# Kernel tuning notes

Hardware: AMD Instinct MI355X
Metric: run time of the kernel (lower is better)

The kernel has to match this reference:

```python
import jax, jax.numpy as jnp
import numpy as np

S, L, E, H, V, T, A = 4096, 16, 512, 512, 100000, 64, 50


def setup_inputs() -> dict:
    key = jax.random.key(0)
    ks = jax.random.split(key, 20)
    f32 = jnp.float32
    n = lambda k, shape: jax.random.normal(k, shape, f32) * 0.05
    return {
        "sent_in": jax.random.randint(ks[0], (S,), 0, V),
        "char_in": jax.random.randint(ks[1], (S, L), 0, A),
        "lengths": jax.random.randint(ks[2], (S,), 1, L + 1),
        "word_emb": n(ks[3], (V, E)),
        "char_emb": n(ks[4], (A, E)),
        "Wih_w": n(ks[5], (4 * H, E)),
        "Whh_w": n(ks[6], (4 * H, H)),
        "bih_w": n(ks[7], (4 * H,)),
        "bhh_w": n(ks[8], (4 * H,)),
        "Wih_c": n(ks[9], (4 * H, E)),
        "Whh_c": n(ks[10], (4 * H, H)),
        "bih_c": n(ks[11], (4 * H,)),
        "bhh_c": n(ks[12], (4 * H,)),
        "Ww2t": n(ks[13], (T, H)),
        "bw2t": n(ks[14], (T,)),
        "Wc2t": n(ks[15], (T, H)),
        "bc2t": n(ks[16], (T,)),
    }


def _lstm(xs, mask, W_ih, W_hh, b_ih, b_hh):
    """xs: [T, B, E], mask: [T, B] (1 = valid). Returns hs: [T, B, H].
    PyTorch gate order i, f, g, o. Carry is frozen on masked steps."""
    Hd = W_hh.shape[1]
    B = xs.shape[1]
    gx = jnp.einsum('tbe,ge->tbg', xs, W_ih) + b_ih  # precompute input gates

    def step(carry, inp):
        h, c = carry
        g, m = inp
        gates = g + h @ W_hh.T + b_hh
        i, f, gg, o = jnp.split(gates, 4, axis=-1)
        c_new = jax.nn.sigmoid(f) * c + jax.nn.sigmoid(i) * jnp.tanh(gg)
        h_new = jax.nn.sigmoid(o) * jnp.tanh(c_new)
        mm = m[:, None]
        h_new = jnp.where(mm, h_new, h)
        c_new = jnp.where(mm, c_new, c)
        return (h_new, c_new), h_new

    h0 = jnp.zeros((B, Hd), xs.dtype)
    c0 = jnp.zeros((B, Hd), xs.dtype)
    _, hs = jax.lax.scan(step, (h0, c0), (gx, mask))
    return hs


def reference(sent_in, char_in, lengths, word_emb, char_emb,
              Wih_w, Whh_w, bih_w, bhh_w,
              Wih_c, Whh_c, bih_c, bhh_c,
              Ww2t, bw2t, Wc2t, bc2t):
    # word-level LSTM over the sentence (batch = 1)
    xs_w = word_emb[sent_in][:, None, :]                  # [S, 1, E]
    mask_w = jnp.ones((sent_in.shape[0], 1), jnp.bool_)
    hs_w = _lstm(xs_w, mask_w, Wih_w, Whh_w, bih_w, bhh_w)  # [S, 1, H]
    word_scores = hs_w[:, 0, :] @ Ww2t.T + bw2t           # [S, T]

    # char-level LSTM: all words processed as one batch, masked by length
    xs_c = char_emb[char_in].transpose(1, 0, 2)           # [L, S, E]
    Lm = char_in.shape[1]
    mask_c = jnp.arange(Lm)[:, None] < lengths[None, :]   # [L, S]
    hs_c = _lstm(xs_c, mask_c, Wih_c, Whh_c, bih_c, bhh_c)  # [L, S, H]
    out_sum = jnp.sum(hs_c * mask_c[:, :, None].astype(hs_c.dtype), axis=0)  # [S, H]
    char_scores = out_sum @ Wc2t.T + bc2t                 # [S, T]

    return jax.nn.log_softmax(char_scores + word_scores, axis=1)
```

## Files before the change

kernel.cpp:

```cpp
#include <hip/hip_runtime.h>
#include <cstdint>
#include <cstddef>

#define S_  4096
#define L_  16
#define E_  512
#define H_  512
#define G4_ 2048
#define T_  64
#define WORD_WGS 32
#define CHAR_WGS 256
#define ALL_WGS  (WORD_WGS + CHAR_WGS)

__device__ __forceinline__ float sigmoidf_(float x) {
    return 1.0f / (1.0f + __expf(-x));
}
__device__ __forceinline__ float fast_tanhf_(float x) {
    return 1.0f - 2.0f / (__expf(2.0f * x) + 1.0f);
}

#define BM 128
#define BN 128
#define BK 16

__global__ __launch_bounds__(256, 2)
void gemm_nt_kernel(const float* __restrict__ A1, const int* __restrict__ idxA,
                    int idxStride, int idxOff, const float* __restrict__ A2,
                    const float* __restrict__ B1, const float* __restrict__ B2,
                    int Ksplit, int K, int N, float* __restrict__ C)
{
    __shared__ float As_[BK][BM + 4];
    __shared__ float Bs_[BK][BN + 4];
    __shared__ int   rIdx_[BM];

    const int tid = threadIdx.x;
    const int m0 = blockIdx.y * BM;
    const int n0 = blockIdx.x * BN;
    if (idxA && tid < BM)
        rIdx_[tid] = idxA[(size_t)(m0 + tid) * idxStride + idxOff];

    const int tx = tid & 15;
    const int ty = tid >> 4;
    const int ar = tid >> 2;
    const int aq = tid & 3;

    float acc[8][8];
#pragma unroll
    for (int i = 0; i < 8; ++i)
#pragma unroll
        for (int j = 0; j < 8; ++j) acc[i][j] = 0.f;

    for (int k0 = 0; k0 < K; k0 += BK) {
        __syncthreads();
        const bool firstHalf = (k0 < Ksplit);
        const int  kk0 = firstHalf ? k0 : (k0 - Ksplit);
#pragma unroll
        for (int part = 0; part < 2; ++part) {
            const int row = ar + part * 64;
            float4 av, bv;
            if (firstHalf) {
                const int grA = idxA ? rIdx_[row] : (m0 + row);
                av = *(const float4*)(A1 + (size_t)grA * Ksplit + kk0 + aq * 4);
                bv = *(const float4*)(B1 + (size_t)(n0 + row) * Ksplit + kk0 + aq * 4);
            } else {
                const int Kr = K - Ksplit;
                av = *(const float4*)(A2 + (size_t)(m0 + row) * Kr + kk0 + aq * 4);
                bv = *(const float4*)(B2 + (size_t)(n0 + row) * Kr + kk0 + aq * 4);
            }
            As_[aq * 4 + 0][row] = av.x; As_[aq * 4 + 1][row] = av.y;
            As_[aq * 4 + 2][row] = av.z; As_[aq * 4 + 3][row] = av.w;
            Bs_[aq * 4 + 0][row] = bv.x; Bs_[aq * 4 + 1][row] = bv.y;
            Bs_[aq * 4 + 2][row] = bv.z; Bs_[aq * 4 + 3][row] = bv.w;
        }
        __syncthreads();
#pragma unroll
        for (int kk = 0; kk < BK; ++kk) {
            const float4 a0 = *(const float4*)&As_[kk][ty * 4];
            const float4 a1 = *(const float4*)&As_[kk][64 + ty * 4];
            const float4 b0 = *(const float4*)&Bs_[kk][tx * 4];
            const float4 b1 = *(const float4*)&Bs_[kk][64 + tx * 4];
            const float a[8] = {a0.x, a0.y, a0.z, a0.w, a1.x, a1.y, a1.z, a1.w};
            const float b[8] = {b0.x, b0.y, b0.z, b0.w, b1.x, b1.y, b1.z, b1.w};
#pragma unroll
            for (int i = 0; i < 8; ++i)
#pragma unroll
                for (int j = 0; j < 8; ++j)
                    acc[i][j] = fmaf(a[i], b[j], acc[i][j]);
        }
    }
#pragma unroll
    for (int ri = 0; ri < 2; ++ri)
#pragma unroll
        for (int i = 0; i < 4; ++i) {
            const int m = m0 + ri * 64 + ty * 4 + i;
            float4 v0 = make_float4(acc[ri * 4 + i][0], acc[ri * 4 + i][1],
                                    acc[ri * 4 + i][2], acc[ri * 4 + i][3]);
            float4 v1 = make_float4(acc[ri * 4 + i][4], acc[ri * 4 + i][5],
                                    acc[ri * 4 + i][6], acc[ri * 4 + i][7]);
            *(float4*)(C + (size_t)m * N + n0 + tx * 4)      = v0;
            *(float4*)(C + (size_t)m * N + n0 + 64 + tx * 4) = v1;
        }
}

__global__ __launch_bounds__(512, 4)
void fused_lstm_kernel(const float* __restrict__ gxw,
                       const float* __restrict__ Whh_w,
                       const float* __restrict__ bih_w,
                       const float* __restrict__ bhh_w,
                       float* __restrict__ hsw, float* __restrict__ h_buf,
                       unsigned int* __restrict__ cnt,
                       const int* __restrict__ char_in,
                       const int* __restrict__ lengths,
                       const float* __restrict__ char_emb,
                       const float* __restrict__ Wih_c,
                       const float* __restrict__ Whh_c,
                       const float* __restrict__ bih_c,
                       const float* __restrict__ bhh_c,
                       float* __restrict__ h_c, float* __restrict__ c_c,
                       float* __restrict__ osum)
{
    __shared__ float h_lds[512];
    __shared__ float gate_lds[64];
    __shared__ float wb[64];
    __shared__ float As[16][132];
    __shared__ float Bs[16][260];
    __shared__ int   rIdx[128];
    __shared__ int   lens[128];
    __shared__ float cb[256];

    const int tid = threadIdx.x;

    if (blockIdx.x < WORD_WGS) {
        const int wg   = blockIdx.x;
        const int base = wg * 16;
        const int r    = tid >> 3;
        const int p    = tid & 7;
        const int grow = (r >> 4) * 512 + base + (r & 15);

        float wreg[64];
        {
            const float4* Wrow = (const float4*)(Whh_w + (size_t)grow * 512);
#pragma unroll
            for (int kk = 0; kk < 16; ++kk) {
                const float4 v = Wrow[kk * 8 + p];
                wreg[kk * 4 + 0] = v.x; wreg[kk * 4 + 1] = v.y;
                wreg[kk * 4 + 2] = v.z; wreg[kk * 4 + 3] = v.w;
            }
#pragma unroll
            for (int i = 0; i < 64; ++i) asm volatile("" : "+v"(wreg[i]));
        }
        if (tid < 64) {
            const int gr = (tid >> 4) * 512 + base + (tid & 15);
            wb[tid] = bih_w[gr] + bhh_w[gr];
        }
        if (tid < 128) ((float4*)h_lds)[tid] = make_float4(0.f, 0.f, 0.f, 0.f);
        float cstate = 0.f;
        __syncthreads();

        float gxv = (p == 0) ? gxw[grow] : 0.f;
        for (int t = 0; t < S_; ++t) {
            float gxn = 0.f;
            if (p == 0 && t + 1 < S_) gxn = gxw[(size_t)(t + 1) * G4_ + grow];

            float s = 0.f;
#pragma unroll
            for (int kk = 0; kk < 16; ++kk) {
                const float4 h4 = ((const float4*)h_lds)[kk * 8 + p];
                s = fmaf(wreg[kk * 4 + 0], h4.x, s);
                s = fmaf(wreg[kk * 4 + 1], h4.y, s);
                s = fmaf(wreg[kk * 4 + 2], h4.z, s);
                s = fmaf(wreg[kk * 4 + 3], h4.w, s);
            }
            s += __shfl_xor(s, 1);
            s += __shfl_xor(s, 2);
            s += __shfl_xor(s, 4);
            if (p == 0) gate_lds[r] = s + gxv + wb[r];
            __syncthreads();

            if (tid < 16) {
                const float gi = gate_lds[tid];
                const float gf = gate_lds[16 + tid];
                const float gg = gate_lds[32 + tid];
                const float go = gate_lds[48 + tid];
                const float cn = sigmoidf_(gf) * cstate + sigmoidf_(gi) * fast_tanhf_(gg);
                cstate = cn;
                const float hn = sigmoidf_(go) * fast_tanhf_(cn);
                hsw[(size_t)t * H_ + base + tid] = hn;
                __hip_atomic_store(&h_buf[((t + 1) & 1) * H_ + base + tid], hn,
                                   __ATOMIC_RELAXED, __HIP_MEMORY_SCOPE_AGENT);
            }
            __syncthreads();

            if (tid == 0) {
                __hip_atomic_fetch_add(&cnt[0], 1u, __ATOMIC_RELEASE,
                                       __HIP_MEMORY_SCOPE_AGENT);
                while (__hip_atomic_load(&cnt[0], __ATOMIC_ACQUIRE,
                                         __HIP_MEMORY_SCOPE_AGENT)
                       < (unsigned)WORD_WGS * (unsigned)(t + 1))
                    __builtin_amdgcn_s_sleep(2);
            }
            __syncthreads();

            h_lds[tid] = __hip_atomic_load(&h_buf[((t + 1) & 1) * H_ + tid],
                                           __ATOMIC_RELAXED, __HIP_MEMORY_SCOPE_AGENT);
            __syncthreads();
            gxv = gxn;
        }
    } else {
        const int cw  = blockIdx.x - WORD_WGS;
        const int m0  = (cw >> 3) * 128;
        const int hu0 = (cw & 7) * 64;
        const int tx  = tid & 31;
        const int ty  = tid >> 5;

        if (tid < 128) lens[tid] = lengths[m0 + tid];
        if (tid < 256) {
            const int g = tid >> 6, ul = tid & 63;
            const int br = g * 512 + hu0 + ul;
            cb[tid] = bih_c[br] + bhh_c[br];
        }

        for (int l = 0; l < L_; ++l) {
            if (tid < 128) rIdx[tid] = char_in[(size_t)(m0 + tid) * L_ + l];

            float acc[8][8];
#pragma unroll
            for (int i = 0; i < 8; ++i)
#pragma unroll
                for (int j = 0; j < 8; ++j) acc[i][j] = 0.f;

            for (int kt = 0; kt < 64; ++kt) {
                const int k0 = kt * 16;
                __syncthreads();
                const int row = tid >> 2, q = tid & 3;
                float4 av;
                if (k0 < 512) {
                    av = *(const float4*)(char_emb + (size_t)rIdx[row] * E_ + k0 + q * 4);
                } else {
                    const float* hp = h_c + (size_t)(m0 + row) * H_ + (k0 - 512) + q * 4;
                    av.x = __hip_atomic_load(hp + 0, __ATOMIC_RELAXED, __HIP_MEMORY_SCOPE_AGENT);
                    av.y = __hip_atomic_load(hp + 1, __ATOMIC_RELAXED, __HIP_MEMORY_SCOPE_AGENT);
                    av.z = __hip_atomic_load(hp + 2, __ATOMIC_RELAXED, __HIP_MEMORY_SCOPE_AGENT);
                    av.w = __hip_atomic_load(hp + 3, __ATOMIC_RELAXED, __HIP_MEMORY_SCOPE_AGENT);
                }
                As[q * 4 + 0][row] = av.x; As[q * 4 + 1][row] = av.y;
                As[q * 4 + 2][row] = av.z; As[q * 4 + 3][row] = av.w;
#pragma unroll
                for (int cc = 0; cc < 2; ++cc) {
                    const int c  = row + cc * 128;
                    const int g  = c >> 6, u = c & 63;
                    const int br = g * 512 + hu0 + u;
                    const float* bp = (k0 < 512)
                        ? (Wih_c + (size_t)br * E_ + k0 + q * 4)
                        : (Whh_c + (size_t)br * H_ + (k0 - 512) + q * 4);
                    const float4 bv = *(const float4*)bp;
                    Bs[q * 4 + 0][c] = bv.x; Bs[q * 4 + 1][c] = bv.y;
                    Bs[q * 4 + 2][c] = bv.z; Bs[q * 4 + 3][c] = bv.w;
                }
                __syncthreads();
#pragma unroll
                for (int kk = 0; kk < 16; ++kk) {
                    const float4 a0 = *(const float4*)&As[kk][ty * 8];
                    const float4 a1 = *(const float4*)&As[kk][ty * 8 + 4];
                    const float a[8] = {a0.x, a0.y, a0.z, a0.w, a1.x, a1.y, a1.z, a1.w};
                    float b[8];
#pragma unroll
                    for (int g = 0; g < 4; ++g) {
                        const float2 bg = *(const float2*)&Bs[kk][g * 64 + 2 * tx];
                        b[(g << 1)]     = bg.x;
                        b[(g << 1) | 1] = bg.y;
                    }
#pragma unroll
                    for (int i = 0; i < 8; ++i)
#pragma unroll
                        for (int j = 0; j < 8; ++j)
                            acc[i][j] = fmaf(a[i], b[j], acc[i][j]);
                }
            }

            __syncthreads();
            if (tid == 0) {
                __hip_atomic_fetch_add(&cnt[32], 1u, __ATOMIC_RELEASE,
                                       __HIP_MEMORY_SCOPE_AGENT);
                while (__hip_atomic_load(&cnt[32], __ATOMIC_ACQUIRE,
                                         __HIP_MEMORY_SCOPE_AGENT)
                       < (unsigned)CHAR_WGS * (unsigned)(2 * l + 1))
                    __builtin_amdgcn_s_sleep(2);
            }
            __syncthreads();

#pragma unroll
            for (int i = 0; i < 8; ++i) {
                const int mr = ty * 8 + i;
                const int m  = m0 + mr;
                if (l < lens[mr]) {
                    const int hl = 2 * tx;
                    float* cp = c_c  + (size_t)m * H_ + hu0 + hl;
                    float* op = osum + (size_t)m * H_ + hu0 + hl;
                    float2 c2 = *(float2*)cp;
                    float2 o2 = *(float2*)op;
#pragma unroll
                    for (int u = 0; u < 2; ++u) {
                        const float I = sigmoidf_(acc[i][0 + u] + cb[      hl + u]);
                        const float F = sigmoidf_(acc[i][2 + u] + cb[ 64 + hl + u]);
                        const float G = fast_tanhf_(acc[i][4 + u] + cb[128 + hl + u]);
                        const float O = sigmoidf_(acc[i][6 + u] + cb[192 + hl + u]);
                        const float cv = u ? c2.y : c2.x;
                        const float cn = F * cv + I * G;
                        const float hn = O * fast_tanhf_(cn);
                        if (u) { c2.y = cn; o2.y += hn; } else { c2.x = cn; o2.x += hn; }
                        __hip_atomic_store(h_c + (size_t)m * H_ + hu0 + hl + u, hn,
                                           __ATOMIC_RELAXED, __HIP_MEMORY_SCOPE_AGENT);
                    }
                    *(float2*)cp = c2;
                    *(float2*)op = o2;
                }
            }

            __syncthreads();
            if (tid == 0) {
                __hip_atomic_fetch_add(&cnt[32], 1u, __ATOMIC_RELEASE,
                                       __HIP_MEMORY_SCOPE_AGENT);
                while (__hip_atomic_load(&cnt[32], __ATOMIC_ACQUIRE,
                                         __HIP_MEMORY_SCOPE_AGENT)
                       < (unsigned)CHAR_WGS * (unsigned)(2 * l + 2))
                    __builtin_amdgcn_s_sleep(2);
            }
            __syncthreads();
        }
    }
}

__global__ __launch_bounds__(64)
void scores_kernel(const float* __restrict__ hsw, const float* __restrict__ osum,
                   const float* __restrict__ Ww2t, const float* __restrict__ bw2t,
                   const float* __restrict__ Wc2t, const float* __restrict__ bc2t,
                   float* __restrict__ out)
{
    const int s = blockIdx.x;
    const int t = threadIdx.x;
    __shared__ float4 hrow[128], orow[128];
    hrow[t]      = ((const float4*)(hsw + (size_t)s * H_))[t];
    hrow[t + 64] = ((const float4*)(hsw + (size_t)s * H_))[t + 64];
    orow[t]      = ((const float4*)(osum + (size_t)s * H_))[t];
    orow[t + 64] = ((const float4*)(osum + (size_t)s * H_))[t + 64];
    __syncthreads();

    float acc = bw2t[t] + bc2t[t];
    const float4* w1 = (const float4*)(Ww2t + (size_t)t * H_);
    const float4* w2 = (const float4*)(Wc2t + (size_t)t * H_);
#pragma unroll 8
    for (int k = 0; k < 128; ++k) {
        const float4 a = w1[k], hb = hrow[k];
        acc = fmaf(a.x, hb.x, acc); acc = fmaf(a.y, hb.y, acc);
        acc = fmaf(a.z, hb.z, acc); acc = fmaf(a.w, hb.w, acc);
        const float4 b = w2[k], ob = orow[k];
        acc = fmaf(b.x, ob.x, acc); acc = fmaf(b.y, ob.y, acc);
        acc = fmaf(b.z, ob.z, acc); acc = fmaf(b.w, ob.w, acc);
    }
    float m = acc;
#pragma unroll
    for (int off = 32; off > 0; off >>= 1) m = fmaxf(m, __shfl_xor(m, off));
    float sum = __expf(acc - m);
#pragma unroll
    for (int off = 32; off > 0; off >>= 1) sum += __shfl_xor(sum, off);
    out[(size_t)s * T_ + t] = acc - m - __logf(sum);
}

extern "C" void kernel_launch(void* const* d_in, const int* in_sizes, int n_in,
                              void* d_out, int out_size, void* d_ws, size_t ws_size,
                              hipStream_t stream)
{
    (void)in_sizes; (void)n_in; (void)out_size; (void)ws_size;

    const int*   sent_in  = (const int*)d_in[0];
    const int*   char_in  = (const int*)d_in[1];
    const int*   lengths  = (const int*)d_in[2];
    const float* word_emb = (const float*)d_in[3];
    const float* char_emb = (const float*)d_in[4];
    const float* Wih_w    = (const float*)d_in[5];
    const float* Whh_w    = (const float*)d_in[6];
    const float* bih_w    = (const float*)d_in[7];
    const float* bhh_w    = (const float*)d_in[8];
    const float* Wih_c    = (const float*)d_in[9];
    const float* Whh_c    = (const float*)d_in[10];
    const float* bih_c    = (const float*)d_in[11];
    const float* bhh_c    = (const float*)d_in[12];
    const float* Ww2t     = (const float*)d_in[13];
    const float* bw2t     = (const float*)d_in[14];
    const float* Wc2t     = (const float*)d_in[15];
    const float* bc2t     = (const float*)d_in[16];

    char* ws = (char*)d_ws;
    float* gxw  = (float*)(ws + 0);
    float* hsw  = (float*)(ws + 33554432);
    float* h_c  = (float*)(ws + 41943040);
    float* c_c  = (float*)(ws + 50331648);
    float* osum = (float*)(ws + 58720256);
    float* hbuf = (float*)(ws + 67108864);
    unsigned int* cnt = (unsigned int*)(ws + 67112960);

    hipMemsetAsync(hbuf, 0, 4096, stream);
    hipMemsetAsync(cnt,  0, 16384, stream);
    hipMemsetAsync(h_c,  0, 8388608, stream);
    hipMemsetAsync(c_c,  0, 8388608, stream);
    hipMemsetAsync(osum, 0, 8388608, stream);

    const dim3 gemmGrid(G4_ / BN, S_ / BM);
    gemm_nt_kernel<<<gemmGrid, 256, 0, stream>>>(
        word_emb, sent_in, 1, 0, nullptr,
        Wih_w, nullptr, E_, E_, G4_, gxw);

    fused_lstm_kernel<<<ALL_WGS, 512, 0, stream>>>(
        gxw, Whh_w, bih_w, bhh_w, hsw, hbuf, cnt,
        char_in, lengths, char_emb, Wih_c, Whh_c, bih_c, bhh_c,
        h_c, c_c, osum);

    scores_kernel<<<S_, 64, 0, stream>>>(hsw, osum, Ww2t, bw2t, Wc2t, bc2t,
                                         (float*)d_out);
}
```

Measured before the change: 14.88 ms.

## Spread word LSTM over 128 workgroups with per-workgroup flag barrier

```diff
diff --git a/kernel.cpp b/kernel.cpp
--- a/kernel.cpp
+++ b/kernel.cpp
@@ -8,8 +8,8 @@
 #define H_  512
 #define G4_ 2048
 #define T_  64
-#define WORD_WGS 32
-#define CHAR_WGS 256
+#define WORD_WGS 128
+#define CHAR_WGS 128
 #define ALL_WGS  (WORD_WGS + CHAR_WGS)
 
 __device__ __forceinline__ float sigmoidf_(float x) {
@@ -25,9 +25,9 @@
 
 __global__ __launch_bounds__(256, 2)
 void gemm_nt_kernel(const float* __restrict__ A1, const int* __restrict__ idxA,
-                    int idxStride, int idxOff, const float* __restrict__ A2,
-                    const float* __restrict__ B1, const float* __restrict__ B2,
-                    int Ksplit, int K, int N, float* __restrict__ C)
+                    int idxStride, int idxOff,
+                    const float* __restrict__ B1, int K, int N,
+                    float* __restrict__ C)
 {
     __shared__ float As_[BK][BM + 4];
     __shared__ float Bs_[BK][BN + 4];
@@ -36,7 +36,7 @@
     const int tid = threadIdx.x;
     const int m0 = blockIdx.y * BM;
     const int n0 = blockIdx.x * BN;
-    if (idxA && tid < BM)
+    if (tid < BM)
         rIdx_[tid] = idxA[(size_t)(m0 + tid) * idxStride + idxOff];
 
     const int tx = tid & 15;
@@ -52,21 +52,12 @@
 
     for (int k0 = 0; k0 < K; k0 += BK) {
         __syncthreads();
-        const bool firstHalf = (k0 < Ksplit);
-        const int  kk0 = firstHalf ? k0 : (k0 - Ksplit);
 #pragma unroll
         for (int part = 0; part < 2; ++part) {
             const int row = ar + part * 64;
-            float4 av, bv;
-            if (firstHalf) {
-                const int grA = idxA ? rIdx_[row] : (m0 + row);
-                av = *(const float4*)(A1 + (size_t)grA * Ksplit + kk0 + aq * 4);
-                bv = *(const float4*)(B1 + (size_t)(n0 + row) * Ksplit + kk0 + aq * 4);
-            } else {
-                const int Kr = K - Ksplit;
-                av = *(const float4*)(A2 + (size_t)(m0 + row) * Kr + kk0 + aq * 4);
-                bv = *(const float4*)(B2 + (size_t)(n0 + row) * Kr + kk0 + aq * 4);
-            }
+            const int grA = rIdx_[row];
+            float4 av = *(const float4*)(A1 + (size_t)grA * K + k0 + aq * 4);
+            float4 bv = *(const float4*)(B1 + (size_t)(n0 + row) * K + k0 + aq * 4);
             As_[aq * 4 + 0][row] = av.x; As_[aq * 4 + 1][row] = av.y;
             As_[aq * 4 + 2][row] = av.z; As_[aq * 4 + 3][row] = av.w;
             Bs_[aq * 4 + 0][row] = bv.x; Bs_[aq * 4 + 1][row] = bv.y;
@@ -119,101 +110,111 @@
                        float* __restrict__ h_c, float* __restrict__ c_c,
                        float* __restrict__ osum)
 {
-    __shared__ float h_lds[512];
-    __shared__ float gate_lds[64];
-    __shared__ float wb[64];
-    __shared__ float As[16][132];
-    __shared__ float Bs[16][260];
-    __shared__ int   rIdx[128];
-    __shared__ int   lens[128];
-    __shared__ float cb[256];
-
+    __shared__ __align__(16) unsigned char smem[27392];
     const int tid = threadIdx.x;
 
     if (blockIdx.x < WORD_WGS) {
+        float* h_lds    = (float*)smem;
+        float* gate_lds = (float*)(smem + 2048);
+        float* wb       = (float*)(smem + 2112);
+
         const int wg   = blockIdx.x;
-        const int base = wg * 16;
-        const int r    = tid >> 3;
-        const int p    = tid & 7;
-        const int grow = (r >> 4) * 512 + base + (r & 15);
-
-        float wreg[64];
+        const int base = wg * 4;
+        const int r    = tid >> 5;
+        const int p    = tid & 31;
+        const int grow = (r >> 2) * 512 + base + (r & 3);
+
+        float4 w0, w1, w2, w3;
         {
             const float4* Wrow = (const float4*)(Whh_w + (size_t)grow * 512);
-#pragma unroll
-            for (int kk = 0; kk < 16; ++kk) {
-                const float4 v = Wrow[kk * 8 + p];
-                wreg[kk * 4 + 0] = v.x; wreg[kk * 4 + 1] = v.y;
-                wreg[kk * 4 + 2] = v.z; wreg[kk * 4 + 3] = v.w;
-            }
-#pragma unroll
-            for (int i = 0; i < 64; ++i) asm volatile("" : "+v"(wreg[i]));
-        }
-        if (tid < 64) {
-            const int gr = (tid >> 4) * 512 + base + (tid & 15);
+            w0 = Wrow[p];       w1 = Wrow[32 + p];
+            w2 = Wrow[64 + p];  w3 = Wrow[96 + p];
+        }
+        if (tid < 16) {
+            const int gr = (tid >> 2) * 512 + base + (tid & 3);
             wb[tid] = bih_w[gr] + bhh_w[gr];
         }
         if (tid < 128) ((float4*)h_lds)[tid] = make_float4(0.f, 0.f, 0.f, 0.f);
         float cstate = 0.f;
         __syncthreads();
 
+        unsigned int* flags = cnt + 64;
         float gxv = (p == 0) ? gxw[grow] : 0.f;
+
         for (int t = 0; t < S_; ++t) {
             float gxn = 0.f;
             if (p == 0 && t + 1 < S_) gxn = gxw[(size_t)(t + 1) * G4_ + grow];
 
+            const float4* h4 = (const float4*)h_lds;
+            float4 ha = h4[p], hb = h4[32 + p], hc = h4[64 + p], hd = h4[96 + p];
             float s = 0.f;
-#pragma unroll
-            for (int kk = 0; kk < 16; ++kk) {
-                const float4 h4 = ((const float4*)h_lds)[kk * 8 + p];
-                s = fmaf(wreg[kk * 4 + 0], h4.x, s);
-                s = fmaf(wreg[kk * 4 + 1], h4.y, s);
-                s = fmaf(wreg[kk * 4 + 2], h4.z, s);
-                s = fmaf(wreg[kk * 4 + 3], h4.w, s);
-            }
+            s = fmaf(w0.x, ha.x, s); s = fmaf(w0.y, ha.y, s);
+            s = fmaf(w0.z, ha.z, s); s = fmaf(w0.w, ha.w, s);
+            s = fmaf(w1.x, hb.x, s); s = fmaf(w1.y, hb.y, s);
+            s = fmaf(w1.z, hb.z, s); s = fmaf(w1.w, hb.w, s);
+            s = fmaf(w2.x, hc.x, s); s = fmaf(w2.y, hc.y, s);
+            s = fmaf(w2.z, hc.z, s); s = fmaf(w2.w, hc.w, s);
+            s = fmaf(w3.x, hd.x, s); s = fmaf(w3.y, hd.y, s);
+            s = fmaf(w3.z, hd.z, s); s = fmaf(w3.w, hd.w, s);
+            s += __shfl_xor(s, 16);
+            s += __shfl_xor(s, 8);
+            s += __shfl_xor(s, 4);
+            s += __shfl_xor(s, 2);
             s += __shfl_xor(s, 1);
-            s += __shfl_xor(s, 2);
-            s += __shfl_xor(s, 4);
             if (p == 0) gate_lds[r] = s + gxv + wb[r];
             __syncthreads();
 
-            if (tid < 16) {
-                const float gi = gate_lds[tid];
-                const float gf = gate_lds[16 + tid];
-                const float gg = gate_lds[32 + tid];
-                const float go = gate_lds[48 + tid];
-                const float cn = sigmoidf_(gf) * cstate + sigmoidf_(gi) * fast_tanhf_(gg);
-                cstate = cn;
-                const float hn = sigmoidf_(go) * fast_tanhf_(cn);
-                hsw[(size_t)t * H_ + base + tid] = hn;
-                __hip_atomic_store(&h_buf[((t + 1) & 1) * H_ + base + tid], hn,
-                                   __ATOMIC_RELAXED, __HIP_MEMORY_SCOPE_AGENT);
+            if (tid < 64) {
+                if (tid < 4) {
+                    const float gi = gate_lds[tid];
+                    const float gf = gate_lds[4 + tid];
+                    const float gg = gate_lds[8 + tid];
+                    const float go = gate_lds[12 + tid];
+                    const float cn = sigmoidf_(gf) * cstate
+                                   + sigmoidf_(gi) * fast_tanhf_(gg);
+                    cstate = cn;
+                    const float hn = sigmoidf_(go) * fast_tanhf_(cn);
+                    hsw[(size_t)t * H_ + base + tid] = hn;
+                    __hip_atomic_store(&h_buf[((t + 1) & 1) * H_ + base + tid],
+                                       hn, __ATOMIC_RELAXED,
+                                       __HIP_MEMORY_SCOPE_AGENT);
+                }
+                if (tid == 0)
+                    __hip_atomic_store(&flags[wg * 16],
+                                       (unsigned int)(t + 1), __ATOMIC_RELEASE,
+                                       __HIP_MEMORY_SCOPE_AGENT);
+                const unsigned int tp1 = (unsigned int)(t + 1);
+                for (;;) {
+                    unsigned int f1 = __hip_atomic_load(
+                        &flags[tid * 16], __ATOMIC_ACQUIRE,
+                        __HIP_MEMORY_SCOPE_AGENT);
+                    unsigned int f2 = __hip_atomic_load(
+                        &flags[(64 + tid) * 16], __ATOMIC_ACQUIRE,
+                        __HIP_MEMORY_SCOPE_AGENT);
+                    if (__all((int)(f1 >= tp1 && f2 >= tp1))) break;
+                    __builtin_amdgcn_s_sleep(1);
+                }
             }
             __syncthreads();
-
-            if (tid == 0) {
-                __hip_atomic_fetch_add(&cnt[0], 1u, __ATOMIC_RELEASE,
-                                       __HIP_MEMORY_SCOPE_AGENT);
-                while (__hip_atomic_load(&cnt[0], __ATOMIC_ACQUIRE,
-                                         __HIP_MEMORY_SCOPE_AGENT)
-                       < (unsigned)WORD_WGS * (unsigned)(t + 1))
-                    __builtin_amdgcn_s_sleep(2);
-            }
-            __syncthreads();
-
             h_lds[tid] = __hip_atomic_load(&h_buf[((t + 1) & 1) * H_ + tid],
-                                           __ATOMIC_RELAXED, __HIP_MEMORY_SCOPE_AGENT);
+                                           __ATOMIC_RELAXED,
+                                           __HIP_MEMORY_SCOPE_AGENT);
             __syncthreads();
             gxv = gxn;
         }
     } else {
-        const int cw  = blockIdx.x - WORD_WGS;
-        const int m0  = (cw >> 3) * 128;
-        const int hu0 = (cw & 7) * 64;
-        const int tx  = tid & 31;
-        const int ty  = tid >> 5;
-
-        if (tid < 128) lens[tid] = lengths[m0 + tid];
+        float (*As)[132] = (float(*)[132])smem;
+        float (*Bs)[260] = (float(*)[260])(smem + 8448);
+        int*   rIdx = (int*)(smem + 25088);
+        int*   lens = (int*)(smem + 25600);
+        float* cb   = (float*)(smem + 26112);
+
+        const int cw   = blockIdx.x - WORD_WGS;
+        const int mgrp = cw >> 3;
+        const int hu0  = (cw & 7) * 64;
+        const int tx   = tid & 31;
+        const int ty   = tid >> 5;
+
         if (tid < 256) {
             const int g = tid >> 6, ul = tid & 63;
             const int br = g * 512 + hu0 + ul;
@@ -221,112 +222,124 @@
         }
 
         for (int l = 0; l < L_; ++l) {
-            if (tid < 128) rIdx[tid] = char_in[(size_t)(m0 + tid) * L_ + l];
-
-            float acc[8][8];
-#pragma unroll
-            for (int i = 0; i < 8; ++i)
-#pragma unroll
-                for (int j = 0; j < 8; ++j) acc[i][j] = 0.f;
-
-            for (int kt = 0; kt < 64; ++kt) {
-                const int k0 = kt * 16;
+            for (int mt = 0; mt < 2; ++mt) {
+                const int m0 = (mgrp + mt * 16) * 128;
+                const unsigned int ph = (unsigned int)((l * 2 + mt) * 2);
+                if (tid < 128) {
+                    rIdx[tid] = char_in[(size_t)(m0 + tid) * L_ + l];
+                    lens[tid] = lengths[m0 + tid];
+                }
+
+                float acc[8][8];
+#pragma unroll
+                for (int i = 0; i < 8; ++i)
+#pragma unroll
+                    for (int j = 0; j < 8; ++j) acc[i][j] = 0.f;
+
+                for (int kt = 0; kt < 64; ++kt) {
+                    const int k0 = kt * 16;
+                    __syncthreads();
+                    const int row = tid >> 2, q = tid & 3;
+                    float4 av;
+                    if (k0 < 512) {
+                        av = *(const float4*)(char_emb
+                             + (size_t)rIdx[row] * E_ + k0 + q * 4);
+                    } else {
+                        const float* hp = h_c + (size_t)(m0 + row) * H_
+                                        + (k0 - 512) + q * 4;
+                        av.x = __hip_atomic_load(hp + 0, __ATOMIC_RELAXED, __HIP_MEMORY_SCOPE_AGENT);
+                        av.y = __hip_atomic_load(hp + 1, __ATOMIC_RELAXED, __HIP_MEMORY_SCOPE_AGENT);
+                        av.z = __hip_atomic_load(hp + 2, __ATOMIC_RELAXED, __HIP_MEMORY_SCOPE_AGENT);
+                        av.w = __hip_atomic_load(hp + 3, __ATOMIC_RELAXED, __HIP_MEMORY_SCOPE_AGENT);
+                    }
+                    As[q * 4 + 0][row] = av.x; As[q * 4 + 1][row] = av.y;
+                    As[q * 4 + 2][row] = av.z; As[q * 4 + 3][row] = av.w;
+#pragma unroll
+                    for (int cc = 0; cc < 2; ++cc) {
+                        const int c  = row + cc * 128;
+                        const int g  = c >> 6, u = c & 63;
+                        const int br = g * 512 + hu0 + u;
+                        const float* bp = (k0 < 512)
+                            ? (Wih_c + (size_t)br * E_ + k0 + q * 4)
+                            : (Whh_c + (size_t)br * H_ + (k0 - 512) + q * 4);
+                        const float4 bv = *(const float4*)bp;
+                        Bs[q * 4 + 0][c] = bv.x; Bs[q * 4 + 1][c] = bv.y;
+                        Bs[q * 4 + 2][c] = bv.z; Bs[q * 4 + 3][c] = bv.w;
+                    }
+                    __syncthreads();
+#pragma unroll
+                    for (int kk = 0; kk < 16; ++kk) {
+                        const float4 a0 = *(const float4*)&As[kk][ty * 8];
+                        const float4 a1 = *(const float4*)&As[kk][ty * 8 + 4];
+                        const float a[8] = {a0.x, a0.y, a0.z, a0.w,
+                                            a1.x, a1.y, a1.z, a1.w};
+                        float b[8];
+#pragma unroll
+                        for (int g = 0; g < 4; ++g) {
+                            const float2 bg = *(const float2*)&Bs[kk][g * 64 + 2 * tx];
+                            b[(g << 1)]     = bg.x;
+                            b[(g << 1) | 1] = bg.y;
+                        }
+#pragma unroll
+                        for (int i = 0; i < 8; ++i)
+#pragma unroll
+                            for (int j = 0; j < 8; ++j)
+                                acc[i][j] = fmaf(a[i], b[j], acc[i][j]);
+                    }
+                }
+
                 __syncthreads();
-                const int row = tid >> 2, q = tid & 3;
-                float4 av;
-                if (k0 < 512) {
-                    av = *(const float4*)(char_emb + (size_t)rIdx[row] * E_ + k0 + q * 4);
-                } else {
-                    const float* hp = h_c + (size_t)(m0 + row) * H_ + (k0 - 512) + q * 4;
-                    av.x = __hip_atomic_load(hp + 0, __ATOMIC_RELAXED, __HIP_MEMORY_SCOPE_AGENT);
-                    av.y = __hip_atomic_load(hp + 1, __ATOMIC_RELAXED, __HIP_MEMORY_SCOPE_AGENT);
-                    av.z = __hip_atomic_load(hp + 2, __ATOMIC_RELAXED, __HIP_MEMORY_SCOPE_AGENT);
-                    av.w = __hip_atomic_load(hp + 3, __ATOMIC_RELAXED, __HIP_MEMORY_SCOPE_AGENT);
-                }
-                As[q * 4 + 0][row] = av.x; As[q * 4 + 1][row] = av.y;
-                As[q * 4 + 2][row] = av.z; As[q * 4 + 3][row] = av.w;
-#pragma unroll
-                for (int cc = 0; cc < 2; ++cc) {
-                    const int c  = row + cc * 128;
-                    const int g  = c >> 6, u = c & 63;
-                    const int br = g * 512 + hu0 + u;
-                    const float* bp = (k0 < 512)
-                        ? (Wih_c + (size_t)br * E_ + k0 + q * 4)
-                        : (Whh_c + (size_t)br * H_ + (k0 - 512) + q * 4);
-                    const float4 bv = *(const float4*)bp;
-                    Bs[q * 4 + 0][c] = bv.x; Bs[q * 4 + 1][c] = bv.y;
-                    Bs[q * 4 + 2][c] = bv.z; Bs[q * 4 + 3][c] = bv.w;
+                if (tid == 0) {
+                    __hip_atomic_fetch_add(&cnt[0], 1u, __ATOMIC_RELEASE,
+                                           __HIP_MEMORY_SCOPE_AGENT);
+                    while (__hip_atomic_load(&cnt[0], __ATOMIC_ACQUIRE,
+                                             __HIP_MEMORY_SCOPE_AGENT)
+                           < (unsigned)CHAR_WGS * (ph + 1))
+                        __builtin_amdgcn_s_sleep(2);
                 }
                 __syncthreads();
-#pragma unroll
-                for (int kk = 0; kk < 16; ++kk) {
-                    const float4 a0 = *(const float4*)&As[kk][ty * 8];
-                    const float4 a1 = *(const float4*)&As[kk][ty * 8 + 4];
-                    const float a[8] = {a0.x, a0.y, a0.z, a0.w, a1.x, a1.y, a1.z, a1.w};
-                    float b[8];
-#pragma unroll
-                    for (int g = 0; g < 4; ++g) {
-                        const float2 bg = *(const float2*)&Bs[kk][g * 64 + 2 * tx];
-                        b[(g << 1)]     = bg.x;
-                        b[(g << 1) | 1] = bg.y;
+
+#pragma unroll
+                for (int i = 0; i < 8; ++i) {
+                    const int mr = ty * 8 + i;
+                    const int m  = m0 + mr;
+                    if (l < lens[mr]) {
+                        const int hl = 2 * tx;
+                        float* cp = c_c  + (size_t)m * H_ + hu0 + hl;
+                        float* op = osum + (size_t)m * H_ + hu0 + hl;
+                        float2 c2 = *(float2*)cp;
+                        float2 o2 = *(float2*)op;
+#pragma unroll
+                        for (int u = 0; u < 2; ++u) {
+                            const float I = sigmoidf_(acc[i][0 + u] + cb[      hl + u]);
+                            const float F = sigmoidf_(acc[i][2 + u] + cb[ 64 + hl + u]);
+                            const float G = fast_tanhf_(acc[i][4 + u] + cb[128 + hl + u]);
+                            const float O = sigmoidf_(acc[i][6 + u] + cb[192 + hl + u]);
+                            const float cv = u ? c2.y : c2.x;
+                            const float cn = F * cv + I * G;
+                            const float hn = O * fast_tanhf_(cn);
+                            if (u) { c2.y = cn; o2.y += hn; }
+                            else   { c2.x = cn; o2.x += hn; }
+                            __hip_atomic_store(h_c + (size_t)m * H_ + hu0 + hl + u,
+                                               hn, __ATOMIC_RELAXED,
+                                               __HIP_MEMORY_SCOPE_AGENT);
+                        }
+                        *(float2*)cp = c2;
+                        *(float2*)op = o2;
                     }
-#pragma unroll
-                    for (int i = 0; i < 8; ++i)
-#pragma unroll
-                        for (int j = 0; j < 8; ++j)
-                            acc[i][j] = fmaf(a[i], b[j], acc[i][j]);
-                }
+                }
+
+                __syncthreads();
+                if (tid == 0) {
+                    __hip_atomic_fetch_add(&cnt[0], 1u, __ATOMIC_RELEASE,
+                                           __HIP_MEMORY_SCOPE_AGENT);
+                    while (__hip_atomic_load(&cnt[0], __ATOMIC_ACQUIRE,
+                                             __HIP_MEMORY_SCOPE_AGENT)
+                           < (unsigned)CHAR_WGS * (ph + 2))
+                        __builtin_amdgcn_s_sleep(2);
+                }
+                __syncthreads();
             }
-
-            __syncthreads();
-            if (tid == 0) {
-                __hip_atomic_fetch_add(&cnt[32], 1u, __ATOMIC_RELEASE,
-                                       __HIP_MEMORY_SCOPE_AGENT);
-                while (__hip_atomic_load(&cnt[32], __ATOMIC_ACQUIRE,
-                                         __HIP_MEMORY_SCOPE_AGENT)
-                       < (unsigned)CHAR_WGS * (unsigned)(2 * l + 1))
-                    __builtin_amdgcn_s_sleep(2);
-            }
-            __syncthreads();
-
-#pragma unroll
-            for (int i = 0; i < 8; ++i) {
-                const int mr = ty * 8 + i;
-                const int m  = m0 + mr;
-                if (l < lens[mr]) {
-                    const int hl = 2 * tx;
-                    float* cp = c_c  + (size_t)m * H_ + hu0 + hl;
-                    float* op = osum + (size_t)m * H_ + hu0 + hl;
-                    float2 c2 = *(float2*)cp;
-                    float2 o2 = *(float2*)op;
-#pragma unroll
-                    for (int u = 0; u < 2; ++u) {
-                        const float I = sigmoidf_(acc[i][0 + u] + cb[      hl + u]);
-                        const float F = sigmoidf_(acc[i][2 + u] + cb[ 64 + hl + u]);
-                        const float G = fast_tanhf_(acc[i][4 + u] + cb[128 + hl + u]);
-                        const float O = sigmoidf_(acc[i][6 + u] + cb[192 + hl + u]);
-                        const float cv = u ? c2.y : c2.x;
-                        const float cn = F * cv + I * G;
-                        const float hn = O * fast_tanhf_(cn);
-                        if (u) { c2.y = cn; o2.y += hn; } else { c2.x = cn; o2.x += hn; }
-                        __hip_atomic_store(h_c + (size_t)m * H_ + hu0 + hl + u, hn,
-                                           __ATOMIC_RELAXED, __HIP_MEMORY_SCOPE_AGENT);
-                    }
-                    *(float2*)cp = c2;
-                    *(float2*)op = o2;
-                }
-            }
-
-            __syncthreads();
-            if (tid == 0) {
-                __hip_atomic_fetch_add(&cnt[32], 1u, __ATOMIC_RELEASE,
-                                       __HIP_MEMORY_SCOPE_AGENT);
-                while (__hip_atomic_load(&cnt[32], __ATOMIC_ACQUIRE,
-                                         __HIP_MEMORY_SCOPE_AGENT)
-                       < (unsigned)CHAR_WGS * (unsigned)(2 * l + 2))
-                    __builtin_amdgcn_s_sleep(2);
-            }
-            __syncthreads();
         }
     }
 }
@@ -408,8 +421,8 @@
 
     const dim3 gemmGrid(G4_ / BN, S_ / BM);
     gemm_nt_kernel<<<gemmGrid, 256, 0, stream>>>(
-        word_emb, sent_in, 1, 0, nullptr,
-        Wih_w, nullptr, E_, E_, G4_, gxw);
+        word_emb, sent_in, 1, 0,
+        Wih_w, E_, G4_, gxw);
 
     fused_lstm_kernel<<<ALL_WGS, 512, 0, stream>>>(
         gxw, Whh_w, bih_w, bhh_w, hsw, hbuf, cnt,
```

New measurement: 31.32 ms. 110% more time.
